# Optimization experiments

Measured on AMD Instinct MI355X. Metric: run time of the kernel, lower is better.

The kernel has to match this reference:

```python
import jax, jax.numpy as jnp
import numpy as np

WS = 7       # window size
SHIFT = 3    # shift size
NH = 6       # num heads

def layernorm(x, w, b, eps=1e-5):
    mu = jnp.mean(x, axis=-1, keepdims=True)
    var = jnp.var(x, axis=-1, keepdims=True)
    return (x - mu) * jax.lax.rsqrt(var + eps) * w + b

def setup_inputs() -> dict:
    key = jax.random.key(0)
    ks = jax.random.split(key, 8)
    B, H, W, C = 16, 56, 56, 192
    hid = 4 * C
    s = lambda k, shape, fan: jax.random.normal(k, shape, jnp.float32) * (fan ** -0.5)
    return {
        "x": jax.random.normal(ks[0], (B, H, W, C), jnp.float32),
        "ln1_w": jnp.ones((C,), jnp.float32), "ln1_b": jnp.zeros((C,), jnp.float32),
        "qkv_w": s(ks[1], (C, 3 * C), C), "qkv_b": jnp.zeros((3 * C,), jnp.float32),
        "proj_w": s(ks[2], (C, C), C), "proj_b": jnp.zeros((C,), jnp.float32),
        "ln2_w": jnp.ones((C,), jnp.float32), "ln2_b": jnp.zeros((C,), jnp.float32),
        "mlp_w1": s(ks[3], (C, hid), C), "mlp_b1": jnp.zeros((hid,), jnp.float32),
        "mlp_w2": s(ks[4], (hid, C), hid), "mlp_b2": jnp.zeros((C,), jnp.float32),
    }

def reference(x, ln1_w, ln1_b, qkv_w, qkv_b, proj_w, proj_b, ln2_w, ln2_b, mlp_w1, mlp_b1, mlp_w2, mlp_b2):
    B, H, W, C = x.shape
    hd = C // NH
    scale = hd ** -0.5
    N = WS * WS

    shortcut = x
    xn = layernorm(x, ln1_w, ln1_b)
    # cyclic shift
    xs = jnp.roll(xn, shift=(-SHIFT, -SHIFT), axis=(1, 2))
    # window partition: [B*nW, N, C]
    xw = xs.reshape(B, H // WS, WS, W // WS, WS, C)
    xw = xw.transpose(0, 1, 3, 2, 4, 5).reshape(-1, N, C)

    # window attention
    qkv = xw @ qkv_w + qkv_b                       # [Bn, N, 3C]
    qkv = qkv.reshape(-1, N, 3, NH, hd).transpose(2, 0, 3, 1, 4)  # [3, Bn, NH, N, hd]
    q, k, v = qkv[0], qkv[1], qkv[2]
    attn = jnp.einsum('bhqd,bhkd->bhqk', q, k) * scale
    attn = jax.nn.softmax(attn, axis=-1)
    o = jnp.einsum('bhqk,bhkd->bhqd', attn, v)     # [Bn, NH, N, hd]
    o = o.transpose(0, 2, 1, 3).reshape(-1, N, C)
    o = o @ proj_w + proj_b

    # window reverse
    o = o.reshape(B, H // WS, W // WS, WS, WS, C)
    o = o.transpose(0, 1, 3, 2, 4, 5).reshape(B, H, W, C)
    # reverse shift
    o = jnp.roll(o, shift=(SHIFT, SHIFT), axis=(1, 2))

    x = shortcut + o
    # MLP (exact GELU, matching torch nn.GELU default)
    h = layernorm(x, ln2_w, ln2_b)
    h = jax.nn.gelu(h @ mlp_w1 + mlp_b1, approximate=False)
    x = x + (h @ mlp_w2 + mlp_b2)
    return x
```

## Files before the change

### kernel.cpp

```cpp
#include <hip/hip_runtime.h>
#include <hip/hip_bf16.h>
#include <math.h>

typedef __attribute__((ext_vector_type(8))) short short8;
typedef __attribute__((ext_vector_type(4))) float float4v;
typedef __attribute__((ext_vector_type(2))) unsigned int uint2v;

#define C_DIM 192
#define NHEADS 6
#define NTOK 50176

__device__ __forceinline__ float bf2f(unsigned short u){
  union { unsigned int i; float f; } x; x.i = ((unsigned int)u) << 16; return x.f;
}
__device__ __forceinline__ unsigned short f2bf(float f){
  union { float f; unsigned int i; } x; x.f = f;
  unsigned int r = x.i + 0x7fff + ((x.i >> 16) & 1);
  return (unsigned short)(r >> 16);
}
__device__ __forceinline__ unsigned int rbf(float f){
  union { float f; unsigned int i; } x; x.f = f;
  return x.i + 0x7fff + ((x.i >> 16) & 1);
}
__device__ __forceinline__ unsigned int pack_bf2(float lo, float hi){
  return __builtin_amdgcn_perm(rbf(hi), rbf(lo), 0x07060302);
}

__device__ __forceinline__ void gload_lds16(const unsigned short* g, unsigned short* l){
  __builtin_amdgcn_global_load_lds((const __attribute__((address_space(1))) void*)g,
                                   (__attribute__((address_space(3))) void*)l, 16, 0, 0);
}

__device__ __forceinline__ int nat_token(int r){
  int win = r / 49, n = r - win * 49;
  int b = win >> 6, rem = win & 63;
  int hs = (rem >> 3) * 7 + n / 7;
  int ws = (rem & 7) * 7 + n % 7;
  int h = hs + 3; if (h >= 56) h -= 56;
  int w = ws + 3; if (w >= 56) w -= 56;
  return (b * 56 + h) * 56 + w;
}

__device__ __forceinline__ float gelu_f(float v){
  float t = v * v;
  float u = fmaf(0.1029436f, t, 2.302208f);
  float e = __builtin_amdgcn_exp2f(-v * u);
  return v * __builtin_amdgcn_rcpf(1.f + e);
}

__global__ void transpose_kernel(const float* __restrict__ in,
                                 unsigned short* __restrict__ out, int R, int Cc){
  int idx = blockIdx.x * 256 + threadIdx.x;
  if (idx < R * Cc){ int r = idx / Cc, c = idx - r * Cc; out[(long)c * R + r] = f2bf(in[idx]); }
}

__global__ __launch_bounds__(256) void ln1_kernel(const float* __restrict__ x,
                                                  const float* __restrict__ w,
                                                  const float* __restrict__ b,
                                                  unsigned short* __restrict__ out){
  int wave = threadIdx.x >> 6, lane = threadIdx.x & 63;
  int r = blockIdx.x * 4 + wave;
  int src = nat_token(r);
  const float* xp = x + (long)src * C_DIM;
  float v0 = xp[lane], v1 = xp[lane + 64], v2 = xp[lane + 128];
  float s = v0 + v1 + v2, s2 = v0*v0 + v1*v1 + v2*v2;
  for (int m = 32; m >= 1; m >>= 1){ s += __shfl_xor(s, m, 64); s2 += __shfl_xor(s2, m, 64); }
  float mean = s * (1.f/192.f);
  float var  = s2 * (1.f/192.f) - mean*mean;
  float rs = rsqrtf(var + 1e-5f);
  unsigned short* op = out + (long)r * C_DIM;
  op[lane]       = f2bf((v0-mean)*rs*w[lane]       + b[lane]);
  op[lane + 64]  = f2bf((v1-mean)*rs*w[lane + 64]  + b[lane + 64]);
  op[lane + 128] = f2bf((v2-mean)*rs*w[lane + 128] + b[lane + 128]);
}

__global__ __launch_bounds__(256) void ln2_kernel(const float* __restrict__ y,
                                                  const float* __restrict__ w,
                                                  const float* __restrict__ b,
                                                  unsigned short* __restrict__ out){
  int wave = threadIdx.x >> 6, lane = threadIdx.x & 63;
  int r = blockIdx.x * 4 + wave;
  const float* yp = y + (long)r * C_DIM;
  float v0 = yp[lane], v1 = yp[lane + 64], v2 = yp[lane + 128];
  float s = v0 + v1 + v2, s2 = v0*v0 + v1*v1 + v2*v2;
  for (int m = 32; m >= 1; m >>= 1){ s += __shfl_xor(s, m, 64); s2 += __shfl_xor(s2, m, 64); }
  float mean = s * (1.f/192.f);
  float var  = s2 * (1.f/192.f) - mean*mean;
  float rs = rsqrtf(var + 1e-5f);
  unsigned short* op = out + (long)r * C_DIM;
  op[lane]       = f2bf((v0-mean)*rs*w[lane]       + b[lane]);
  op[lane + 64]  = f2bf((v1-mean)*rs*w[lane + 64]  + b[lane + 64]);
  op[lane + 128] = f2bf((v2-mean)*rs*w[lane + 128] + b[lane + 128]);
}

__global__ __launch_bounds__(256) void attn_kernel(const unsigned short* __restrict__ qkv,
                                                   unsigned short* __restrict__ o){
  __shared__ unsigned short pbuf[4][64][72];
  int wave = threadIdx.x >> 6, lane = threadIdx.x & 63;
  int quad = lane >> 4, l16 = lane & 15;
  int wid = blockIdx.x * 4 + wave;
  int win = wid / NHEADS, head = wid - win * NHEADS;
  const unsigned short* qp = qkv + (long)win * 49 * 576 + head * 32;
  const unsigned short* kp = qp + 192;
  const unsigned short* vp = qp + 384;

  short8 qa[4], kb[4];
  #pragma unroll
  for (int mi = 0; mi < 4; mi++){
    int m = mi * 16 + l16; if (m > 48) m = 48;
    qa[mi] = *(const short8*)&qp[(long)m * 576 + quad * 8];
  }
  #pragma unroll
  for (int ni = 0; ni < 4; ni++){
    int n = ni * 16 + l16; if (n > 48) n = 48;
    kb[ni] = *(const short8*)&kp[(long)n * 576 + quad * 8];
  }
  float4v S[4][4];
  #pragma unroll
  for (int mi = 0; mi < 4; mi++)
    #pragma unroll
    for (int ni = 0; ni < 4; ni++) S[mi][ni] = (float4v)0.f;
  #pragma unroll
  for (int mi = 0; mi < 4; mi++)
    #pragma unroll
    for (int ni = 0; ni < 4; ni++)
      S[mi][ni] = __builtin_amdgcn_mfma_f32_16x16x32_bf16(qa[mi], kb[ni], S[mi][ni], 0, 0, 0);

  #pragma unroll
  for (int mi = 0; mi < 4; mi++){
    #pragma unroll
    for (int r = 0; r < 4; r++){
      float e[4];
      float sum = 0.f;
      #pragma unroll
      for (int ni = 0; ni < 4; ni++){
        int n = ni * 16 + l16;
        float s = S[mi][ni][r] * 0.17677669529663687f;
        s = fminf(s, 80.f);
        float ev = (n <= 48) ? __expf(s) : 0.f;
        e[ni] = ev; sum += ev;
      }
      sum += __shfl_xor(sum, 1, 64);
      sum += __shfl_xor(sum, 2, 64);
      sum += __shfl_xor(sum, 4, 64);
      sum += __shfl_xor(sum, 8, 64);
      float inv = 1.f / sum;
      int m = mi * 16 + quad * 4 + r;
      #pragma unroll
      for (int ni = 0; ni < 4; ni++)
        pbuf[wave][m][ni * 16 + l16] = f2bf(e[ni] * inv);
    }
  }
  __syncthreads();

  short8 vb[2][2];
  #pragma unroll
  for (int kk2 = 0; kk2 < 2; kk2++){
    #pragma unroll
    for (int ni = 0; ni < 2; ni++){
      union { unsigned short us[8]; short8 v8; } u;
      #pragma unroll
      for (int j = 0; j < 8; j++){
        int k = kk2 * 32 + quad * 8 + j; if (k > 48) k = 48;
        u.us[j] = vp[(long)k * 576 + ni * 16 + l16];
      }
      vb[kk2][ni] = u.v8;
    }
  }

  float4v O[4][2];
  #pragma unroll
  for (int mi = 0; mi < 4; mi++)
    #pragma unroll
    for (int ni = 0; ni < 2; ni++) O[mi][ni] = (float4v)0.f;
  #pragma unroll
  for (int kk2 = 0; kk2 < 2; kk2++){
    short8 pa[4];
    #pragma unroll
    for (int mi = 0; mi < 4; mi++)
      pa[mi] = *(const short8*)&pbuf[wave][mi * 16 + l16][kk2 * 32 + quad * 8];
    #pragma unroll
    for (int mi = 0; mi < 4; mi++)
      #pragma unroll
      for (int ni = 0; ni < 2; ni++)
        O[mi][ni] = __builtin_amdgcn_mfma_f32_16x16x32_bf16(pa[mi], vb[kk2][ni], O[mi][ni], 0, 0, 0);
  }

  #pragma unroll
  for (int mi = 0; mi < 4; mi++){
    int m0 = mi * 16 + quad * 4;
    #pragma unroll
    for (int r = 0; r < 4; r++){
      if (m0 + r <= 48){
        #pragma unroll
        for (int ni = 0; ni < 2; ni++)
          o[((long)win * 49 + m0 + r) * C_DIM + head * 32 + ni * 16 + l16] = f2bf(O[mi][ni][r]);
      }
    }
  }
}

template<int EPI>
__global__ __launch_bounds__(256) void gemm_kernel(const unsigned short* __restrict__ A,
                                                   const unsigned short* __restrict__ Bt,
                                                   const float* __restrict__ bias,
                                                   unsigned short* __restrict__ Cout,
                                                   float* __restrict__ Fout,
                                                   const float* __restrict__ Xres,
                                                   int N, int K){
  __shared__ unsigned short As[128 * 64];
  __shared__ unsigned short Bs[64 * 64];
  int tid = threadIdx.x;
  int wave = tid >> 6, lane = tid & 63, quad = lane >> 4, l16 = lane & 15;
  int wm = (wave >> 1) * 64, wn = (wave & 1) * 32;
  int lrow = lane >> 3, lg = lane & 7;
  int gcol = (lg ^ lrow) * 8;
  float4v acc[4][2];
  #pragma unroll
  for (int i = 0; i < 4; i++)
    #pragma unroll
    for (int jj = 0; jj < 2; jj++) acc[i][jj] = (float4v)0.f;

  long arow0 = (long)blockIdx.x * 128;
  long brow0 = (long)blockIdx.y * 64;
  int sw = (l16 & 7);

  for (int k0 = 0; k0 < K; k0 += 64){
    #pragma unroll
    for (int t = 0; t < 4; t++){
      int ci = wave + 4 * t;
      gload_lds16(&A[(arow0 + ci * 8 + lrow) * (long)K + k0 + gcol], &As[ci * 512]);
    }
    #pragma unroll
    for (int t = 0; t < 2; t++){
      int ci = wave + 4 * t;
      gload_lds16(&Bt[(brow0 + ci * 8 + lrow) * (long)K + k0 + gcol], &Bs[ci * 512]);
    }
    __syncthreads();
    #pragma unroll
    for (int kk8 = 0; kk8 < 8; kk8 += 4){
      short8 a[4], b[2];
      #pragma unroll
      for (int mi = 0; mi < 4; mi++)
        a[mi] = *(const short8*)&As[(wm + mi*16 + l16) * 64 + ((quad + kk8) ^ sw) * 8];
      #pragma unroll
      for (int ni = 0; ni < 2; ni++)
        b[ni] = *(const short8*)&Bs[(wn + ni*16 + l16) * 64 + ((quad + kk8) ^ sw) * 8];
      #pragma unroll
      for (int mi = 0; mi < 4; mi++)
        #pragma unroll
        for (int ni = 0; ni < 2; ni++)
          acc[mi][ni] = __builtin_amdgcn_mfma_f32_16x16x32_bf16(b[ni], a[mi], acc[mi][ni], 0, 0, 0);
    }
    __syncthreads();
  }

  float4v bias4[2];
  #pragma unroll
  for (int ni = 0; ni < 2; ni++)
    bias4[ni] = *(const float4v*)&bias[brow0 + wn + ni*16 + quad*4];

  #pragma unroll
  for (int mi = 0; mi < 4; mi++){
    long r = arow0 + wm + mi*16 + l16;
    long tr = (EPI == 1) ? (long)nat_token((int)r) : r;
    #pragma unroll
    for (int ni = 0; ni < 2; ni++){
      long c0 = brow0 + wn + ni*16 + quad*4;
      float4v v = acc[mi][ni] + bias4[ni];
      if (EPI == 0 || EPI == 2){
        if (EPI == 2){
          #pragma unroll
          for (int e = 0; e < 4; e++) v[e] = gelu_f(v[e]);
        }
        uint2v pp;
        pp[0] = pack_bf2(v[0], v[1]);
        pp[1] = pack_bf2(v[2], v[3]);
        *(uint2v*)&Cout[r * N + c0] = pp;
      } else {
        long idx = tr * C_DIM + c0;
        float4v xr = *(const float4v*)&Xres[idx];
        *(float4v*)&Fout[idx] = xr + v;
      }
    }
  }
}

extern "C" void kernel_launch(void* const* d_in, const int* in_sizes, int n_in,
                              void* d_out, int out_size, void* d_ws, size_t ws_size,
                              hipStream_t stream){
  const float* x      = (const float*)d_in[0];
  const float* ln1_w  = (const float*)d_in[1];
  const float* ln1_b  = (const float*)d_in[2];
  const float* qkv_w  = (const float*)d_in[3];
  const float* qkv_b  = (const float*)d_in[4];
  const float* proj_w = (const float*)d_in[5];
  const float* proj_b = (const float*)d_in[6];
  const float* ln2_w  = (const float*)d_in[7];
  const float* ln2_b  = (const float*)d_in[8];
  const float* mlp_w1 = (const float*)d_in[9];
  const float* mlp_b1 = (const float*)d_in[10];
  const float* mlp_w2 = (const float*)d_in[11];
  const float* mlp_b2 = (const float*)d_in[12];
  float* out = (float*)d_out;

  char* ws = (char*)d_ws;
  unsigned short* qkv_wt = (unsigned short*)(ws);
  unsigned short* proj_wt= (unsigned short*)(ws + 221184);
  unsigned short* w1t    = (unsigned short*)(ws + 294912);
  unsigned short* w2t    = (unsigned short*)(ws + 589824);
  unsigned short* R1     = (unsigned short*)(ws + 884736);
  unsigned short* R0     = (unsigned short*)(ws + 20152320);

  unsigned short* xw   = R1;
  unsigned short* obuf = R1;
  unsigned short* hn   = R1;
  unsigned short* qkv  = R0;
  unsigned short* hbuf = R0;

  transpose_kernel<<<(110592 + 255) / 256, 256, 0, stream>>>(qkv_w, qkv_wt, 192, 576);
  transpose_kernel<<<(36864  + 255) / 256, 256, 0, stream>>>(proj_w, proj_wt, 192, 192);
  transpose_kernel<<<(147456 + 255) / 256, 256, 0, stream>>>(mlp_w1, w1t, 192, 768);
  transpose_kernel<<<(147456 + 255) / 256, 256, 0, stream>>>(mlp_w2, w2t, 768, 192);

  ln1_kernel<<<NTOK / 4, 256, 0, stream>>>(x, ln1_w, ln1_b, xw);
  gemm_kernel<0><<<dim3(392, 9),  256, 0, stream>>>(xw, qkv_wt, qkv_b, qkv, nullptr, nullptr, 576, 192);
  attn_kernel<<<(NTOK / 49) * NHEADS / 4, 256, 0, stream>>>(qkv, obuf);
  gemm_kernel<1><<<dim3(392, 3),  256, 0, stream>>>(obuf, proj_wt, proj_b, nullptr, out, x, 192, 192);
  ln2_kernel<<<NTOK / 4, 256, 0, stream>>>(out, ln2_w, ln2_b, hn);
  gemm_kernel<2><<<dim3(392, 12), 256, 0, stream>>>(hn, w1t, mlp_b1, hbuf, nullptr, nullptr, 768, 192);
  gemm_kernel<3><<<dim3(392, 3),  256, 0, stream>>>(hbuf, w2t, mlp_b2, nullptr, out, out, 192, 768);
}
```

Measured before the change: 282.6 us.

## Double-buffer LDS tiles in GEMM kernel to overlap global loads with MFMA

After: 286.3 us. Within noise of the previous version (+1.3%).

```diff
diff --git a/kernel.cpp b/kernel.cpp
--- a/kernel.cpp
+++ b/kernel.cpp
@@ -208,8 +208,8 @@
                                                    float* __restrict__ Fout,
                                                    const float* __restrict__ Xres,
                                                    int N, int K){
-  __shared__ unsigned short As[128 * 64];
-  __shared__ unsigned short Bs[64 * 64];
+  __shared__ unsigned short As[2][128 * 64];
+  __shared__ unsigned short Bs[2][64 * 64];
   int tid = threadIdx.x;
   int wave = tid >> 6, lane = tid & 63, quad = lane >> 4, l16 = lane & 15;
   int wm = (wave >> 1) * 64, wn = (wave & 1) * 32;
@@ -224,35 +224,52 @@
   long arow0 = (long)blockIdx.x * 128;
   long brow0 = (long)blockIdx.y * 64;
   int sw = (l16 & 7);
-
-  for (int k0 = 0; k0 < K; k0 += 64){
-    #pragma unroll
-    for (int t = 0; t < 4; t++){
-      int ci = wave + 4 * t;
-      gload_lds16(&A[(arow0 + ci * 8 + lrow) * (long)K + k0 + gcol], &As[ci * 512]);
-    }
-    #pragma unroll
-    for (int t = 0; t < 2; t++){
-      int ci = wave + 4 * t;
-      gload_lds16(&Bt[(brow0 + ci * 8 + lrow) * (long)K + k0 + gcol], &Bs[ci * 512]);
-    }
-    __syncthreads();
+  int nk = K >> 6;
+
+  #pragma unroll
+  for (int t = 0; t < 4; t++){
+    int ci = wave + 4 * t;
+    gload_lds16(&A[(arow0 + ci * 8 + lrow) * (long)K + gcol], &As[0][ci * 512]);
+  }
+  #pragma unroll
+  for (int t = 0; t < 2; t++){
+    int ci = wave + 4 * t;
+    gload_lds16(&Bt[(brow0 + ci * 8 + lrow) * (long)K + gcol], &Bs[0][ci * 512]);
+  }
+  __syncthreads();
+
+  for (int kt = 0; kt < nk; kt++){
+    if (kt + 1 < nk){
+      int nb = (kt + 1) & 1;
+      long k0 = (long)(kt + 1) << 6;
+      #pragma unroll
+      for (int t = 0; t < 4; t++){
+        int ci = wave + 4 * t;
+        gload_lds16(&A[(arow0 + ci * 8 + lrow) * (long)K + k0 + gcol], &As[nb][ci * 512]);
+      }
+      #pragma unroll
+      for (int t = 0; t < 2; t++){
+        int ci = wave + 4 * t;
+        gload_lds16(&Bt[(brow0 + ci * 8 + lrow) * (long)K + k0 + gcol], &Bs[nb][ci * 512]);
+      }
+    }
+    int cb = kt & 1;
     #pragma unroll
     for (int kk8 = 0; kk8 < 8; kk8 += 4){
       short8 a[4], b[2];
       #pragma unroll
       for (int mi = 0; mi < 4; mi++)
-        a[mi] = *(const short8*)&As[(wm + mi*16 + l16) * 64 + ((quad + kk8) ^ sw) * 8];
+        a[mi] = *(const short8*)&As[cb][(wm + mi*16 + l16) * 64 + ((quad + kk8) ^ sw) * 8];
       #pragma unroll
       for (int ni = 0; ni < 2; ni++)
-        b[ni] = *(const short8*)&Bs[(wn + ni*16 + l16) * 64 + ((quad + kk8) ^ sw) * 8];
+        b[ni] = *(const short8*)&Bs[cb][(wn + ni*16 + l16) * 64 + ((quad + kk8) ^ sw) * 8];
       #pragma unroll
       for (int mi = 0; mi < 4; mi++)
         #pragma unroll
         for (int ni = 0; ni < 2; ni++)
           acc[mi][ni] = __builtin_amdgcn_mfma_f32_16x16x32_bf16(b[ni], a[mi], acc[mi][ni], 0, 0, 0);
     }
-    __syncthreads();
+    if (kt + 1 < nk) __syncthreads();
   }
 
   float4v bias4[2];
```

## Fuse proj GEMM with residual and LN2; add 128x128 tile GEMM for MLP1

Applied to the files above, without the earlier changes.

After: 279.2 us. Within noise of the previous version (-1.2%).

```diff
diff --git a/kernel.cpp b/kernel.cpp
--- a/kernel.cpp
+++ b/kernel.cpp
@@ -74,25 +74,6 @@
   op[lane + 128] = f2bf((v2-mean)*rs*w[lane + 128] + b[lane + 128]);
 }
 
-__global__ __launch_bounds__(256) void ln2_kernel(const float* __restrict__ y,
-                                                  const float* __restrict__ w,
-                                                  const float* __restrict__ b,
-                                                  unsigned short* __restrict__ out){
-  int wave = threadIdx.x >> 6, lane = threadIdx.x & 63;
-  int r = blockIdx.x * 4 + wave;
-  const float* yp = y + (long)r * C_DIM;
-  float v0 = yp[lane], v1 = yp[lane + 64], v2 = yp[lane + 128];
-  float s = v0 + v1 + v2, s2 = v0*v0 + v1*v1 + v2*v2;
-  for (int m = 32; m >= 1; m >>= 1){ s += __shfl_xor(s, m, 64); s2 += __shfl_xor(s2, m, 64); }
-  float mean = s * (1.f/192.f);
-  float var  = s2 * (1.f/192.f) - mean*mean;
-  float rs = rsqrtf(var + 1e-5f);
-  unsigned short* op = out + (long)r * C_DIM;
-  op[lane]       = f2bf((v0-mean)*rs*w[lane]       + b[lane]);
-  op[lane + 64]  = f2bf((v1-mean)*rs*w[lane + 64]  + b[lane + 64]);
-  op[lane + 128] = f2bf((v2-mean)*rs*w[lane + 128] + b[lane + 128]);
-}
-
 __global__ __launch_bounds__(256) void attn_kernel(const unsigned short* __restrict__ qkv,
                                                    unsigned short* __restrict__ o){
   __shared__ unsigned short pbuf[4][64][72];
@@ -268,11 +249,7 @@
     for (int ni = 0; ni < 2; ni++){
       long c0 = brow0 + wn + ni*16 + quad*4;
       float4v v = acc[mi][ni] + bias4[ni];
-      if (EPI == 0 || EPI == 2){
-        if (EPI == 2){
-          #pragma unroll
-          for (int e = 0; e < 4; e++) v[e] = gelu_f(v[e]);
-        }
+      if (EPI == 0){
         uint2v pp;
         pp[0] = pack_bf2(v[0], v[1]);
         pp[1] = pack_bf2(v[2], v[3]);
@@ -282,6 +259,188 @@
         float4v xr = *(const float4v*)&Xres[idx];
         *(float4v*)&Fout[idx] = xr + v;
       }
+    }
+  }
+}
+
+__global__ __launch_bounds__(256, 4) void gemm128_kernel(const unsigned short* __restrict__ A,
+                                                         const unsigned short* __restrict__ Bt,
+                                                         const float* __restrict__ bias,
+                                                         unsigned short* __restrict__ Cout,
+                                                         int N, int K){
+  __shared__ unsigned short As[128 * 64];
+  __shared__ unsigned short Bs[128 * 64];
+  int tid = threadIdx.x;
+  int wave = tid >> 6, lane = tid & 63, quad = lane >> 4, l16 = lane & 15;
+  int wm = (wave >> 1) * 64, wn = (wave & 1) * 64;
+  int lrow = lane >> 3, lg = lane & 7;
+  int gcol = (lg ^ lrow) * 8;
+  int sw = (l16 & 7);
+  float4v acc[4][4];
+  #pragma unroll
+  for (int i = 0; i < 4; i++)
+    #pragma unroll
+    for (int jj = 0; jj < 4; jj++) acc[i][jj] = (float4v)0.f;
+
+  long arow0 = (long)blockIdx.x * 128;
+  long brow0 = (long)blockIdx.y * 128;
+
+  for (int k0 = 0; k0 < K; k0 += 64){
+    #pragma unroll
+    for (int t = 0; t < 4; t++){
+      int ci = wave + 4 * t;
+      gload_lds16(&A[(arow0 + ci * 8 + lrow) * (long)K + k0 + gcol], &As[ci * 512]);
+    }
+    #pragma unroll
+    for (int t = 0; t < 4; t++){
+      int ci = wave + 4 * t;
+      gload_lds16(&Bt[(brow0 + ci * 8 + lrow) * (long)K + k0 + gcol], &Bs[ci * 512]);
+    }
+    __syncthreads();
+    #pragma unroll
+    for (int kk8 = 0; kk8 < 8; kk8 += 4){
+      short8 a[4], b[4];
+      #pragma unroll
+      for (int mi = 0; mi < 4; mi++)
+        a[mi] = *(const short8*)&As[(wm + mi*16 + l16) * 64 + ((quad + kk8) ^ sw) * 8];
+      #pragma unroll
+      for (int ni = 0; ni < 4; ni++)
+        b[ni] = *(const short8*)&Bs[(wn + ni*16 + l16) * 64 + ((quad + kk8) ^ sw) * 8];
+      #pragma unroll
+      for (int mi = 0; mi < 4; mi++)
+        #pragma unroll
+        for (int ni = 0; ni < 4; ni++)
+          acc[mi][ni] = __builtin_amdgcn_mfma_f32_16x16x32_bf16(b[ni], a[mi], acc[mi][ni], 0, 0, 0);
+    }
+    __syncthreads();
+  }
+
+  float4v bias4[4];
+  #pragma unroll
+  for (int ni = 0; ni < 4; ni++)
+    bias4[ni] = *(const float4v*)&bias[brow0 + wn + ni*16 + quad*4];
+
+  #pragma unroll
+  for (int mi = 0; mi < 4; mi++){
+    long r = arow0 + wm + mi*16 + l16;
+    #pragma unroll
+    for (int ni = 0; ni < 4; ni++){
+      long c0 = brow0 + wn + ni*16 + quad*4;
+      float4v v = acc[mi][ni] + bias4[ni];
+      #pragma unroll
+      for (int e = 0; e < 4; e++) v[e] = gelu_f(v[e]);
+      uint2v pp;
+      pp[0] = pack_bf2(v[0], v[1]);
+      pp[1] = pack_bf2(v[2], v[3]);
+      *(uint2v*)&Cout[r * N + c0] = pp;
+    }
+  }
+}
+
+__global__ __launch_bounds__(512, 4) void proj_ln2_kernel(const unsigned short* __restrict__ A,
+                                                          const unsigned short* __restrict__ Bt,
+                                                          const float* __restrict__ bias,
+                                                          const float* __restrict__ x,
+                                                          float* __restrict__ y,
+                                                          const float* __restrict__ lnw,
+                                                          const float* __restrict__ lnb,
+                                                          unsigned short* __restrict__ hn){
+  __shared__ unsigned short As[64 * 64];
+  __shared__ unsigned short Bs[192 * 64];
+  __shared__ float lnred[2][2][16][4][2];
+  int tid = threadIdx.x;
+  int wave = tid >> 6, lane = tid & 63, quad = lane >> 4, l16 = lane & 15;
+  int wr = wave >> 2, wc = wave & 3;
+  int lrow = lane >> 3, lg = lane & 7;
+  int gcol = (lg ^ lrow) * 8;
+  int sw = (l16 & 7);
+  long arow0 = (long)blockIdx.x * 64;
+
+  float4v acc[2][3];
+  #pragma unroll
+  for (int i = 0; i < 2; i++)
+    #pragma unroll
+    for (int j = 0; j < 3; j++) acc[i][j] = (float4v)0.f;
+
+  for (int k0 = 0; k0 < 192; k0 += 64){
+    #pragma unroll
+    for (int t = 0; t < 4; t++){
+      int i = wave + 8 * t;
+      if (i < 8){
+        gload_lds16(&A[(arow0 + i * 8 + lrow) * 192 + k0 + gcol], &As[i * 512]);
+      } else {
+        int ci = i - 8;
+        gload_lds16(&Bt[(ci * 8 + lrow) * 192 + k0 + gcol], &Bs[ci * 512]);
+      }
+    }
+    __syncthreads();
+    #pragma unroll
+    for (int kk8 = 0; kk8 < 8; kk8 += 4){
+      short8 a[2], b[3];
+      #pragma unroll
+      for (int mi = 0; mi < 2; mi++)
+        a[mi] = *(const short8*)&As[(wr*32 + mi*16 + l16) * 64 + ((quad + kk8) ^ sw) * 8];
+      #pragma unroll
+      for (int ni = 0; ni < 3; ni++)
+        b[ni] = *(const short8*)&Bs[(wc*48 + ni*16 + l16) * 64 + ((quad + kk8) ^ sw) * 8];
+      #pragma unroll
+      for (int mi = 0; mi < 2; mi++)
+        #pragma unroll
+        for (int ni = 0; ni < 3; ni++)
+          acc[mi][ni] = __builtin_amdgcn_mfma_f32_16x16x32_bf16(b[ni], a[mi], acc[mi][ni], 0, 0, 0);
+    }
+    if (k0 < 128) __syncthreads();
+  }
+
+  float4v bias4[3];
+  #pragma unroll
+  for (int ni = 0; ni < 3; ni++)
+    bias4[ni] = *(const float4v*)&bias[wc*48 + ni*16 + quad*4];
+
+  #pragma unroll
+  for (int mi = 0; mi < 2; mi++){
+    long rwin = arow0 + wr*32 + mi*16 + l16;
+    long t = nat_token((int)rwin);
+    float s = 0.f, s2 = 0.f;
+    #pragma unroll
+    for (int ni = 0; ni < 3; ni++){
+      long idx = t * C_DIM + wc*48 + ni*16 + quad*4;
+      float4v xr = *(const float4v*)&x[idx];
+      float4v v = acc[mi][ni] + bias4[ni] + xr;
+      *(float4v*)&y[idx] = v;
+      acc[mi][ni] = v;
+      #pragma unroll
+      for (int e = 0; e < 4; e++){ s += v[e]; s2 += v[e]*v[e]; }
+    }
+    s  += __shfl_xor(s, 16, 64);  s  += __shfl_xor(s, 32, 64);
+    s2 += __shfl_xor(s2, 16, 64); s2 += __shfl_xor(s2, 32, 64);
+    if (quad == 0){ lnred[wr][mi][l16][wc][0] = s; lnred[wr][mi][l16][wc][1] = s2; }
+  }
+  __syncthreads();
+
+  #pragma unroll
+  for (int mi = 0; mi < 2; mi++){
+    long rwin = arow0 + wr*32 + mi*16 + l16;
+    float S = 0.f, S2 = 0.f;
+    #pragma unroll
+    for (int w = 0; w < 4; w++){ S += lnred[wr][mi][l16][w][0]; S2 += lnred[wr][mi][l16][w][1]; }
+    float mean = S * (1.f/192.f);
+    float var  = S2 * (1.f/192.f) - mean*mean;
+    float rs = rsqrtf(var + 1e-5f);
+    #pragma unroll
+    for (int ni = 0; ni < 3; ni++){
+      int c0 = wc*48 + ni*16 + quad*4;
+      float4v w4 = *(const float4v*)&lnw[c0];
+      float4v b4 = *(const float4v*)&lnb[c0];
+      float4v v = acc[mi][ni];
+      float g0 = (v[0]-mean)*rs*w4[0] + b4[0];
+      float g1 = (v[1]-mean)*rs*w4[1] + b4[1];
+      float g2 = (v[2]-mean)*rs*w4[2] + b4[2];
+      float g3 = (v[3]-mean)*rs*w4[3] + b4[3];
+      uint2v pp;
+      pp[0] = pack_bf2(g0, g1);
+      pp[1] = pack_bf2(g2, g3);
+      *(uint2v*)&hn[rwin * C_DIM + c0] = pp;
     }
   }
 }
@@ -324,10 +483,9 @@
   transpose_kernel<<<(147456 + 255) / 256, 256, 0, stream>>>(mlp_w2, w2t, 768, 192);
 
   ln1_kernel<<<NTOK / 4, 256, 0, stream>>>(x, ln1_w, ln1_b, xw);
-  gemm_kernel<0><<<dim3(392, 9),  256, 0, stream>>>(xw, qkv_wt, qkv_b, qkv, nullptr, nullptr, 576, 192);
+  gemm_kernel<0><<<dim3(392, 9), 256, 0, stream>>>(xw, qkv_wt, qkv_b, qkv, nullptr, nullptr, 576, 192);
   attn_kernel<<<(NTOK / 49) * NHEADS / 4, 256, 0, stream>>>(qkv, obuf);
-  gemm_kernel<1><<<dim3(392, 3),  256, 0, stream>>>(obuf, proj_wt, proj_b, nullptr, out, x, 192, 192);
-  ln2_kernel<<<NTOK / 4, 256, 0, stream>>>(out, ln2_w, ln2_b, hn);
-  gemm_kernel<2><<<dim3(392, 12), 256, 0, stream>>>(hn, w1t, mlp_b1, hbuf, nullptr, nullptr, 768, 192);
-  gemm_kernel<3><<<dim3(392, 3),  256, 0, stream>>>(hbuf, w2t, mlp_b2, nullptr, out, out, 192, 768);
-}
+  proj_ln2_kernel<<<NTOK / 64, 512, 0, stream>>>(obuf, proj_wt, proj_b, x, out, ln2_w, ln2_b, hn);
+  gemm128_kernel<<<dim3(392, 6), 256, 0, stream>>>(hn, w1t, mlp_b1, hbuf, 768, 192);
+  gemm_kernel<1><<<dim3(392, 3), 256, 0, stream>>>(hbuf, w2t, mlp_b2, nullptr, out, out, 192, 768);
+}
```
